# Performance work log

Measured on AMD Instinct MI355X. Metric: run time of the kernel, lower is better.

The kernel has to match this reference:

```python
import jax, jax.numpy as jnp
import numpy as np

DIM = 256
HID = 128


def setup_inputs() -> dict:
    key = jax.random.key(0)
    ks = jax.random.split(key, 10)
    B, T = 8, 2048
    s_in = 1.0 / np.sqrt(DIM)
    s_h = 1.0 / np.sqrt(HID)
    return {
        "x": jax.random.normal(ks[0], (B, T, DIM), jnp.float32),
        "adapt_bias": jax.random.normal(ks[1], (B, T, T), jnp.float32),
        "Wq": jax.random.uniform(ks[2], (HID, DIM), jnp.float32, -s_in, s_in),
        "bq": jax.random.uniform(ks[3], (HID,), jnp.float32, -s_in, s_in),
        "Wk": jax.random.uniform(ks[4], (HID, DIM), jnp.float32, -s_in, s_in),
        "bk": jax.random.uniform(ks[5], (HID,), jnp.float32, -s_in, s_in),
        "Wv": jax.random.uniform(ks[6], (HID, DIM), jnp.float32, -s_in, s_in),
        "bv": jax.random.uniform(ks[7], (HID,), jnp.float32, -s_in, s_in),
        "Wp": jax.random.uniform(ks[8], (DIM, HID), jnp.float32, -s_h, s_h),
        "bp": jax.random.uniform(ks[9], (DIM,), jnp.float32, -s_h, s_h),
    }


def reference(x, adapt_bias, Wq, bq, Wk, bk, Wv, bv, Wp, bp):
    # y = x (default). Q,K,V: [B,T,H]
    Q = jnp.einsum('btd,hd->bth', x, Wq) + bq
    K = jnp.einsum('btd,hd->bth', x, Wk) + bk
    V = jnp.einsum('btd,hd->bth', x, Wv) + bv
    Q_sig = jax.nn.sigmoid(Q)
    ab = jax.nn.softmax(adapt_bias, axis=-1)        # [B,T,T]
    Ksm = jax.nn.softmax(K, axis=1)                 # softmax over time dim
    eab = jnp.exp(ab)                               # [B,T,T]
    eK = jnp.exp(Ksm)                               # [B,T,H]
    num = jnp.einsum('bts,bsh->bth', eab, eK * V)
    den = jnp.einsum('bts,bsh->bth', eab, eK)
    Yt = Q_sig * (num / den)                        # [B,T,H]
    return jnp.einsum('bth,dh->btd', Yt, Wp) + bp   # [B,T,DIM]
```

## Files before the change

### kernel.cpp

```cpp
#include <hip/hip_runtime.h>
#include <hip/hip_bf16.h>

#define B_ 8
#define T_ 2048
#define D_ 256
#define H_ 128

typedef float f32x4 __attribute__((ext_vector_type(4)));
typedef short bf16x8 __attribute__((ext_vector_type(8)));
typedef unsigned short u16x8 __attribute__((ext_vector_type(8)));

__device__ __forceinline__ unsigned short f2bf(float f){
  union { float f; unsigned u; } v; v.f = f;
  unsigned u = v.u;
  unsigned r = (u + 0x7FFFu + ((u >> 16) & 1u)) >> 16;
  return (unsigned short)r;
}

__device__ __forceinline__ float bf2f(unsigned short us){
  union { unsigned u; float f; } v; v.u = ((unsigned)us) << 16; return v.f;
}

#define GLL16(g, l) __builtin_amdgcn_global_load_lds( \
    (const __attribute__((address_space(1))) void*)(g), \
    (__attribute__((address_space(3))) void*)(l), 16, 0, 0)

__device__ __forceinline__ float blk_reduce(float v, bool is_max, float* sbuf){
  for(int o = 32; o > 0; o >>= 1){
    float t = __shfl_xor(v, o);
    v = is_max ? fmaxf(v, t) : (v + t);
  }
  int w = threadIdx.x >> 6;
  __syncthreads();
  if((threadIdx.x & 63) == 0) sbuf[w] = v;
  __syncthreads();
  float r = sbuf[0];
  for(int i = 1; i < 4; i++) r = is_max ? fmaxf(r, sbuf[i]) : (r + sbuf[i]);
  return r;
}

__global__ __launch_bounds__(256) void qkv_kernel(
    const float* __restrict__ x,
    const float* __restrict__ Wq, const float* __restrict__ bq,
    const float* __restrict__ Wk, const float* __restrict__ bk,
    const float* __restrict__ Wv, const float* __restrict__ bv,
    unsigned short* __restrict__ Qsigb, unsigned short* __restrict__ Ktb,
    unsigned short* __restrict__ Vtb)
{
  const int mat = blockIdx.y;
  const int g0  = blockIdx.x * 64;
  const int tid = threadIdx.x;
  const float* W   = (mat == 0) ? Wq : (mat == 1) ? Wk : Wv;
  const float* bia = (mat == 0) ? bq : (mat == 1) ? bk : bv;

  __shared__ __align__(16) short As[64 * 32];
  __shared__ __align__(16) short Ws[128 * 32];
  __shared__ float tbuf[64][129];

  const int w = tid >> 6, lane = tid & 63, rl = lane & 15, kg = lane >> 4;
  f32x4 acc[8];
  for(int i = 0; i < 8; i++) acc[i] = (f32x4){0.f, 0.f, 0.f, 0.f};

  const int c = tid & 31, r8 = tid >> 5;
  for(int kk = 0; kk < 256; kk += 32){
    __syncthreads();
    for(int p = 0; p < 8; p++){
      int rr = r8 + p * 8;
      As[rr * 32 + c] = (short)f2bf(x[(size_t)(g0 + rr) * 256 + kk + c]);
    }
    for(int p = 0; p < 16; p++){
      int hh = r8 + p * 8;
      Ws[hh * 32 + c] = (short)f2bf(W[(size_t)hh * 256 + kk + c]);
    }
    __syncthreads();
    bf16x8 a = *(const bf16x8*)&As[(w * 16 + rl) * 32 + kg * 8];
    for(int cf = 0; cf < 8; cf++){
      bf16x8 bb = *(const bf16x8*)&Ws[(cf * 16 + rl) * 32 + kg * 8];
      acc[cf] = __builtin_amdgcn_mfma_f32_16x16x32_bf16(a, bb, acc[cf], 0, 0, 0);
    }
  }

  const int b = g0 >> 11, t0 = g0 & 2047;
  if(mat == 0){
    for(int cf = 0; cf < 8; cf++){
      int h = cf * 16 + rl;
      float bh = bia[h];
      for(int r = 0; r < 4; r++){
        int tl = w * 16 + kg * 4 + r;
        float v = acc[cf][r] + bh;
        Qsigb[(size_t)(g0 + tl) * 128 + h] = f2bf(1.f / (1.f + __expf(-v)));
      }
    }
  } else {
    for(int cf = 0; cf < 8; cf++){
      int h = cf * 16 + rl;
      float bh = bia[h];
      for(int r = 0; r < 4; r++){
        int tl = w * 16 + kg * 4 + r;
        tbuf[tl][h] = acc[cf][r] + bh;
      }
    }
    __syncthreads();
    unsigned short* dst = (mat == 1) ? Ktb : Vtb;
    int h = tid >> 1, part = tid & 1;
    unsigned short* drow = dst + (size_t)(b * 128 + h) * 2048 + t0 + part * 32;
#pragma unroll
    for(int i = 0; i < 32; i += 8){
      u16x8 o;
#pragma unroll
      for(int j = 0; j < 8; j++) o[j] = f2bf(tbuf[part * 32 + i + j][h]);
      *(u16x8*)(drow + i) = o;
    }
  }
}

__global__ __launch_bounds__(256) void colsm_kernel(
    const unsigned short* __restrict__ Ktb, const unsigned short* __restrict__ Vtb,
    unsigned short* __restrict__ Mt)
{
  __shared__ float sbuf[4];
  const int b  = blockIdx.x >> 5;
  const int hg = blockIdx.x & 31;
  const int tid = threadIdx.x;
  for(int i = 0; i < 4; i++){
    int h = hg * 4 + i;
    const unsigned short* kr = Ktb + (size_t)(b * 128 + h) * 2048;
    const unsigned short* vr = Vtb + (size_t)(b * 128 + h) * 2048;
    u16x8 k8 = *(const u16x8*)(kr + tid * 8);
    u16x8 v8 = *(const u16x8*)(vr + tid * 8);
    float kf[8];
#pragma unroll
    for(int j = 0; j < 8; j++) kf[j] = bf2f(k8[j]);
    float m = kf[0];
#pragma unroll
    for(int j = 1; j < 8; j++) m = fmaxf(m, kf[j]);
    m = blk_reduce(m, true, sbuf);
    float s = 0.f;
#pragma unroll
    for(int j = 0; j < 8; j++) s += __expf(kf[j] - m);
    s = blk_reduce(s, false, sbuf);
    float iz = 1.f / s;
    u16x8 pv, pe;
#pragma unroll
    for(int j = 0; j < 8; j++){
      float e = __expf(__expf(kf[j] - m) * iz);
      pv[j] = f2bf(e * bf2f(v8[j]));
      pe[j] = f2bf(e);
    }
    *(u16x8*)(Mt + (size_t)(b * 256 + h) * 2048 + tid * 8) = pv;
    *(u16x8*)(Mt + (size_t)(b * 256 + 128 + h) * 2048 + tid * 8) = pe;
  }
}

__global__ __launch_bounds__(256) void softexp_kernel(
    const float* __restrict__ ab, unsigned short* __restrict__ eab)
{
  __shared__ float sbuf[4];
  const size_t row = blockIdx.x;
  const float* r = ab + row * 2048;
  const int tid = threadIdx.x;
  float4 v0 = *(const float4*)(r + tid * 4);
  float4 v1 = *(const float4*)(r + tid * 4 + 1024);
  float m = fmaxf(fmaxf(fmaxf(v0.x, v0.y), fmaxf(v0.z, v0.w)),
                  fmaxf(fmaxf(v1.x, v1.y), fmaxf(v1.z, v1.w)));
  m = blk_reduce(m, true, sbuf);
  float e0x = __expf(v0.x - m), e0y = __expf(v0.y - m);
  float e0z = __expf(v0.z - m), e0w = __expf(v0.w - m);
  float e1x = __expf(v1.x - m), e1y = __expf(v1.y - m);
  float e1z = __expf(v1.z - m), e1w = __expf(v1.w - m);
  float s = e0x + e0y + e0z + e0w + e1x + e1y + e1z + e1w;
  s = blk_reduce(s, false, sbuf);
  float iz = 1.f / s;
  ushort4 o;
  o.x = f2bf(__expf(e0x * iz)); o.y = f2bf(__expf(e0y * iz));
  o.z = f2bf(__expf(e0z * iz)); o.w = f2bf(__expf(e0w * iz));
  *(ushort4*)(eab + row * 2048 + tid * 4) = o;
  o.x = f2bf(__expf(e1x * iz)); o.y = f2bf(__expf(e1y * iz));
  o.z = f2bf(__expf(e1z * iz)); o.w = f2bf(__expf(e1w * iz));
  *(ushort4*)(eab + row * 2048 + tid * 4 + 1024) = o;
}

__global__ __launch_bounds__(256) void aft_gemm4(
    const unsigned short* __restrict__ eab,
    const unsigned short* __restrict__ Mt,
    const unsigned short* __restrict__ Qsigb,
    unsigned short* __restrict__ Yt)
{
  __shared__ __align__(16) unsigned short As2[2][64 * 64];
  __shared__ __align__(16) unsigned short Bs2[2][128 * 64];

  const int bid = blockIdx.x;
  const int b   = bid & 7;
  const int idx = bid >> 3;
  const int rt  = idx >> 1;
  const int hb  = idx & 1;
  const int t0  = rt * 64;
  const int h0  = hb * 64;

  const int tid = threadIdx.x;
  const int w = tid >> 6, lane = tid & 63;
  const int rl = lane & 15, kg = lane >> 4;
  const int wr = w >> 1, wc = w & 1;

  const int lr = lane >> 3;
  const int cc = (lane & 7) ^ lr;

  const size_t rowbase = (size_t)b * 2048 + t0;
  const unsigned short* a_src = eab + (rowbase + (size_t)(w * 16 + lr)) * 2048 + cc * 8;
  const int mtrow = (w < 2) ? (h0 + w * 32 + lr) : (128 + h0 + (w - 2) * 32 + lr);
  const unsigned short* b_src = Mt + ((size_t)b * 256 + mtrow) * 2048 + cc * 8;

  f32x4 acc[2][4];
#pragma unroll
  for(int i = 0; i < 2; i++)
#pragma unroll
    for(int j = 0; j < 4; j++) acc[i][j] = (f32x4){0.f, 0.f, 0.f, 0.f};

  auto stage = [&](int buf, int t){
#pragma unroll
    for(int i = 0; i < 2; i++)
      GLL16(a_src + (size_t)i * 8 * 2048 + t * 64, &As2[buf][(w * 16 + i * 8) * 64]);
#pragma unroll
    for(int i = 0; i < 4; i++)
      GLL16(b_src + (size_t)i * 8 * 2048 + t * 64, &Bs2[buf][(w * 32 + i * 8) * 64]);
  };

  const int rx = rl & 7;
  stage(0, 0);
  stage(1, 1);

  for(int t = 0; t < 32; ++t){
    const int cur = t & 1;
    if(t < 31) asm volatile("s_waitcnt vmcnt(6)" ::: "memory");
    else       asm volatile("s_waitcnt vmcnt(0)" ::: "memory");
    __builtin_amdgcn_s_barrier();
    asm volatile("" ::: "memory");

    bf16x8 af[2][2], bfr[2][4];
#pragma unroll
    for(int ks = 0; ks < 2; ++ks){
      const int slot = ((ks * 4 + kg) ^ rx) * 8;
      af[ks][0] = *(const bf16x8*)&As2[cur][(wr * 32 + rl) * 64 + slot];
      af[ks][1] = *(const bf16x8*)&As2[cur][(wr * 32 + 16 + rl) * 64 + slot];
#pragma unroll
      for(int cf = 0; cf < 4; ++cf){
        const int brow = ((cf < 2) ? (wc * 32 + cf * 16)
                                   : (64 + wc * 32 + (cf - 2) * 16)) + rl;
        bfr[ks][cf] = *(const bf16x8*)&Bs2[cur][brow * 64 + slot];
      }
    }
    asm volatile("s_waitcnt lgkmcnt(0)" ::: "memory");
    __builtin_amdgcn_sched_barrier(0);
    __builtin_amdgcn_s_barrier();
    asm volatile("" ::: "memory");

    if(t < 30) stage(cur, t + 2);

    __builtin_amdgcn_s_setprio(1);
#pragma unroll
    for(int ks = 0; ks < 2; ++ks)
#pragma unroll
      for(int cf = 0; cf < 4; ++cf){
        acc[0][cf] = __builtin_amdgcn_mfma_f32_16x16x32_bf16(af[ks][0], bfr[ks][cf], acc[0][cf], 0, 0, 0);
        acc[1][cf] = __builtin_amdgcn_mfma_f32_16x16x32_bf16(af[ks][1], bfr[ks][cf], acc[1][cf], 0, 0, 0);
      }
    __builtin_amdgcn_s_setprio(0);
  }

#pragma unroll
  for(int rf = 0; rf < 2; ++rf)
#pragma unroll
    for(int cf = 0; cf < 2; ++cf){
      const int h = h0 + wc * 32 + cf * 16 + rl;
#pragma unroll
      for(int r = 0; r < 4; ++r){
        const int tl = wr * 32 + rf * 16 + kg * 4 + r;
        const size_t g = rowbase + tl;
        float num = acc[rf][cf][r], den = acc[rf][cf + 2][r];
        float q = bf2f(Qsigb[g * 128 + h]);
        Yt[g * 128 + h] = f2bf(q * num / den);
      }
    }
}

__global__ __launch_bounds__(256) void outproj_kernel(
    const unsigned short* __restrict__ Yt, const float* __restrict__ Wp,
    const float* __restrict__ bp, float* __restrict__ out)
{
  __shared__ __align__(16) short As[64 * 32];
  __shared__ __align__(16) short Bs[256 * 32];
  const int g0 = blockIdx.x * 64;
  const int tid = threadIdx.x;
  const int w = tid >> 6, lane = tid & 63, rl = lane & 15, kg = lane >> 4;
  f32x4 acc[16];
  for(int i = 0; i < 16; i++) acc[i] = (f32x4){0.f, 0.f, 0.f, 0.f};

  const int ar = tid >> 2, apart = tid & 3;
  const int c = tid & 31, dr = tid >> 5;
  for(int k = 0; k < 128; k += 32){
    __syncthreads();
    *(uint4*)&As[ar * 32 + apart * 8] =
        *(const uint4*)(Yt + (size_t)(g0 + ar) * 128 + k + apart * 8);
    for(int p = 0; p < 32; p++){
      int d = dr + p * 8;
      Bs[d * 32 + c] = (short)f2bf(Wp[(size_t)d * 128 + k + c]);
    }
    __syncthreads();
    bf16x8 a = *(const bf16x8*)&As[(w * 16 + rl) * 32 + kg * 8];
    for(int cf = 0; cf < 16; cf++){
      bf16x8 bb = *(const bf16x8*)&Bs[(cf * 16 + rl) * 32 + kg * 8];
      acc[cf] = __builtin_amdgcn_mfma_f32_16x16x32_bf16(a, bb, acc[cf], 0, 0, 0);
    }
  }
  for(int cf = 0; cf < 16; cf++){
    int d = cf * 16 + rl;
    float bpd = bp[d];
    for(int r = 0; r < 4; r++){
      int tl = w * 16 + kg * 4 + r;
      out[(size_t)(g0 + tl) * 256 + d] = acc[cf][r] + bpd;
    }
  }
}

extern "C" void kernel_launch(void* const* d_in, const int* in_sizes, int n_in,
                              void* d_out, int out_size, void* d_ws, size_t ws_size,
                              hipStream_t stream)
{
  const float* x  = (const float*)d_in[0];
  const float* ab = (const float*)d_in[1];
  const float* Wq = (const float*)d_in[2];
  const float* bq = (const float*)d_in[3];
  const float* Wk = (const float*)d_in[4];
  const float* bk = (const float*)d_in[5];
  const float* Wv = (const float*)d_in[6];
  const float* bv = (const float*)d_in[7];
  const float* Wp = (const float*)d_in[8];
  const float* bp = (const float*)d_in[9];
  float* out = (float*)d_out;

  char* ws = (char*)d_ws;
  unsigned short* Qsigb = (unsigned short*)(ws);
  unsigned short* Ktb   = (unsigned short*)(ws + 8388608);
  unsigned short* Vtb   = (unsigned short*)(ws + 12582912);
  unsigned short* Mt    = (unsigned short*)(ws + 16777216);
  unsigned short* eab   = (unsigned short*)(ws + 25165824);
  unsigned short* Yt    = (unsigned short*)(ws + 8388608);

  qkv_kernel<<<dim3(256, 3), 256, 0, stream>>>(x, Wq, bq, Wk, bk, Wv, bv, Qsigb, Ktb, Vtb);
  colsm_kernel<<<256, 256, 0, stream>>>(Ktb, Vtb, Mt);
  softexp_kernel<<<16384, 256, 0, stream>>>(ab, eab);
  aft_gemm4<<<512, 256, 0, stream>>>(eab, Mt, Qsigb, Yt);
  outproj_kernel<<<256, 256, 0, stream>>>(Yt, Wp, bp, out);
}
```

Measured before the change: 92.94 us.

## Load GEMM operands directly from global into registers, dropping LDS staging

The main attention GEMM no longer stages eab and Mt tiles through LDS with async global-to-LDS loads and barriers. Each wave now loads its MFMA fragments straight from global memory into registers, double-buffered in registers across k-steps, and launch bounds request three blocks per SU. This removes LDS traffic and block-wide synchronisation. In exchange, operands shared between waves are fetched from global or L2 more than once, each lane issues 16-byte loads strided across rows, and register pressure rises.

```diff
diff --git a/kernel.cpp b/kernel.cpp
--- a/kernel.cpp
+++ b/kernel.cpp
@@ -20,10 +20,6 @@
 __device__ __forceinline__ float bf2f(unsigned short us){
   union { unsigned u; float f; } v; v.u = ((unsigned)us) << 16; return v.f;
 }
-
-#define GLL16(g, l) __builtin_amdgcn_global_load_lds( \
-    (const __attribute__((address_space(1))) void*)(g), \
-    (__attribute__((address_space(3))) void*)(l), 16, 0, 0)
 
 __device__ __forceinline__ float blk_reduce(float v, bool is_max, float* sbuf){
   for(int o = 32; o > 0; o >>= 1){
@@ -180,15 +176,12 @@
   *(ushort4*)(eab + row * 2048 + tid * 4 + 1024) = o;
 }
 
-__global__ __launch_bounds__(256) void aft_gemm4(
+__global__ __launch_bounds__(256, 3) void aft_gemm10(
     const unsigned short* __restrict__ eab,
     const unsigned short* __restrict__ Mt,
     const unsigned short* __restrict__ Qsigb,
     unsigned short* __restrict__ Yt)
 {
-  __shared__ __align__(16) unsigned short As2[2][64 * 64];
-  __shared__ __align__(16) unsigned short Bs2[2][128 * 64];
-
   const int bid = blockIdx.x;
   const int b   = bid & 7;
   const int idx = bid >> 3;
@@ -202,13 +195,17 @@
   const int rl = lane & 15, kg = lane >> 4;
   const int wr = w >> 1, wc = w & 1;
 
-  const int lr = lane >> 3;
-  const int cc = (lane & 7) ^ lr;
-
   const size_t rowbase = (size_t)b * 2048 + t0;
-  const unsigned short* a_src = eab + (rowbase + (size_t)(w * 16 + lr)) * 2048 + cc * 8;
-  const int mtrow = (w < 2) ? (h0 + w * 32 + lr) : (128 + h0 + (w - 2) * 32 + lr);
-  const unsigned short* b_src = Mt + ((size_t)b * 256 + mtrow) * 2048 + cc * 8;
+
+  const unsigned short* a_base =
+      eab + (rowbase + (size_t)(wr * 32 + rl)) * 2048 + kg * 8;
+  const unsigned short* b_base[4];
+#pragma unroll
+  for(int cf = 0; cf < 4; cf++){
+    const int colbase = (cf < 2) ? (h0 + wc * 32 + cf * 16)
+                                 : (128 + h0 + wc * 32 + (cf - 2) * 16);
+    b_base[cf] = Mt + ((size_t)b * 256 + colbase + rl) * 2048 + kg * 8;
+  }
 
   f32x4 acc[2][4];
 #pragma unroll
@@ -216,56 +213,38 @@
 #pragma unroll
     for(int j = 0; j < 4; j++) acc[i][j] = (f32x4){0.f, 0.f, 0.f, 0.f};
 
-  auto stage = [&](int buf, int t){
-#pragma unroll
-    for(int i = 0; i < 2; i++)
-      GLL16(a_src + (size_t)i * 8 * 2048 + t * 64, &As2[buf][(w * 16 + i * 8) * 64]);
-#pragma unroll
-    for(int i = 0; i < 4; i++)
-      GLL16(b_src + (size_t)i * 8 * 2048 + t * 64, &Bs2[buf][(w * 32 + i * 8) * 64]);
-  };
-
-  const int rx = rl & 7;
-  stage(0, 0);
-  stage(1, 1);
-
-  for(int t = 0; t < 32; ++t){
-    const int cur = t & 1;
-    if(t < 31) asm volatile("s_waitcnt vmcnt(6)" ::: "memory");
-    else       asm volatile("s_waitcnt vmcnt(0)" ::: "memory");
-    __builtin_amdgcn_s_barrier();
-    asm volatile("" ::: "memory");
-
-    bf16x8 af[2][2], bfr[2][4];
-#pragma unroll
-    for(int ks = 0; ks < 2; ++ks){
-      const int slot = ((ks * 4 + kg) ^ rx) * 8;
-      af[ks][0] = *(const bf16x8*)&As2[cur][(wr * 32 + rl) * 64 + slot];
-      af[ks][1] = *(const bf16x8*)&As2[cur][(wr * 32 + 16 + rl) * 64 + slot];
-#pragma unroll
-      for(int cf = 0; cf < 4; ++cf){
-        const int brow = ((cf < 2) ? (wc * 32 + cf * 16)
-                                   : (64 + wc * 32 + (cf - 2) * 16)) + rl;
-        bfr[ks][cf] = *(const bf16x8*)&Bs2[cur][brow * 64 + slot];
-      }
-    }
-    asm volatile("s_waitcnt lgkmcnt(0)" ::: "memory");
-    __builtin_amdgcn_sched_barrier(0);
-    __builtin_amdgcn_s_barrier();
-    asm volatile("" ::: "memory");
-
-    if(t < 30) stage(cur, t + 2);
-
-    __builtin_amdgcn_s_setprio(1);
-#pragma unroll
-    for(int ks = 0; ks < 2; ++ks)
-#pragma unroll
-      for(int cf = 0; cf < 4; ++cf){
-        acc[0][cf] = __builtin_amdgcn_mfma_f32_16x16x32_bf16(af[ks][0], bfr[ks][cf], acc[0][cf], 0, 0, 0);
-        acc[1][cf] = __builtin_amdgcn_mfma_f32_16x16x32_bf16(af[ks][1], bfr[ks][cf], acc[1][cf], 0, 0, 0);
-      }
-    __builtin_amdgcn_s_setprio(0);
-  }
+  #define LOADT(AB, t) do { \
+    _Pragma("unroll") \
+    for(int ks = 0; ks < 2; ++ks){ \
+      AB##A[ks][0] = *(const bf16x8*)(a_base + (t) * 64 + ks * 32); \
+      AB##A[ks][1] = *(const bf16x8*)(a_base + 16 * 2048 + (t) * 64 + ks * 32); \
+      _Pragma("unroll") \
+      for(int cf = 0; cf < 4; ++cf) \
+        AB##B[ks][cf] = *(const bf16x8*)(b_base[cf] + (t) * 64 + ks * 32); \
+    } \
+  } while(0)
+
+  #define MM(AB) do { \
+    _Pragma("unroll") \
+    for(int ks = 0; ks < 2; ++ks) \
+      _Pragma("unroll") \
+      for(int cf = 0; cf < 4; ++cf){ \
+        acc[0][cf] = __builtin_amdgcn_mfma_f32_16x16x32_bf16(AB##A[ks][0], AB##B[ks][cf], acc[0][cf], 0, 0, 0); \
+        acc[1][cf] = __builtin_amdgcn_mfma_f32_16x16x32_bf16(AB##A[ks][1], AB##B[ks][cf], acc[1][cf], 0, 0, 0); \
+      } \
+  } while(0)
+
+  bf16x8 XA[2][2], XB[2][4], YA[2][2], YB[2][4];
+  LOADT(X, 0);
+#pragma unroll 1
+  for(int t = 0; t < 32; t += 2){
+    LOADT(Y, t + 1);
+    MM(X);
+    if(t + 2 < 32) LOADT(X, t + 2);
+    MM(Y);
+  }
+  #undef LOADT
+  #undef MM
 
 #pragma unroll
   for(int rf = 0; rf < 2; ++rf)
@@ -349,6 +328,6 @@
   qkv_kernel<<<dim3(256, 3), 256, 0, stream>>>(x, Wq, bq, Wk, bk, Wv, bv, Qsigb, Ktb, Vtb);
   colsm_kernel<<<256, 256, 0, stream>>>(Ktb, Vtb, Mt);
   softexp_kernel<<<16384, 256, 0, stream>>>(ab, eab);
-  aft_gemm4<<<512, 256, 0, stream>>>(eab, Mt, Qsigb, Yt);
+  aft_gemm10<<<512, 256, 0, stream>>>(eab, Mt, Qsigb, Yt);
   outproj_kernel<<<256, 256, 0, stream>>>(Yt, Wp, bp, out);
 }
```

Measured after the change: 155.8 us. 1.68x slower.

## Software-pipeline LDS fragment reads against MFMA with register double buffering

Applied to the files above, without the earlier changes.

Restructures the main GEMM loop so the LDS reads for the next k-tile go into a second register set while MFMAs run on the current one, with the loop manually unrolled by two to alternate buffers. It also adds a launch-bounds occupancy hint of 3 blocks per CU. The goal is to hide LDS read latency behind matrix math. The cost is a doubled fragment register footprint, which may conflict with the occupancy hint and cause spills.

```diff
diff --git a/kernel.cpp b/kernel.cpp
--- a/kernel.cpp
+++ b/kernel.cpp
@@ -180,7 +180,7 @@
   *(ushort4*)(eab + row * 2048 + tid * 4 + 1024) = o;
 }
 
-__global__ __launch_bounds__(256) void aft_gemm4(
+__global__ __launch_bounds__(256, 3) void aft_gemm11(
     const unsigned short* __restrict__ eab,
     const unsigned short* __restrict__ Mt,
     const unsigned short* __restrict__ Qsigb,
@@ -226,46 +226,72 @@
   };
 
   const int rx = rl & 7;
+
+  #define DSREAD(BK_, cur) do { \
+    _Pragma("unroll") \
+    for(int ks = 0; ks < 2; ++ks){ \
+      const int slot = ((ks * 4 + kg) ^ rx) * 8; \
+      BK_##A[ks][0] = *(const bf16x8*)&As2[cur][(wr * 32 + rl) * 64 + slot]; \
+      BK_##A[ks][1] = *(const bf16x8*)&As2[cur][(wr * 32 + 16 + rl) * 64 + slot]; \
+      _Pragma("unroll") \
+      for(int cf = 0; cf < 4; ++cf){ \
+        const int brow = ((cf < 2) ? (wc * 32 + cf * 16) \
+                                   : (64 + wc * 32 + (cf - 2) * 16)) + rl; \
+        BK_##B[ks][cf] = *(const bf16x8*)&Bs2[cur][brow * 64 + slot]; \
+      } \
+    } \
+  } while(0)
+
+  #define MM(BK_) do { \
+    __builtin_amdgcn_s_setprio(1); \
+    _Pragma("unroll") \
+    for(int ks = 0; ks < 2; ++ks) \
+      _Pragma("unroll") \
+      for(int cf = 0; cf < 4; ++cf){ \
+        acc[0][cf] = __builtin_amdgcn_mfma_f32_16x16x32_bf16(BK_##A[ks][0], BK_##B[ks][cf], acc[0][cf], 0, 0, 0); \
+        acc[1][cf] = __builtin_amdgcn_mfma_f32_16x16x32_bf16(BK_##A[ks][1], BK_##B[ks][cf], acc[1][cf], 0, 0, 0); \
+      } \
+    __builtin_amdgcn_s_setprio(0); \
+  } while(0)
+
+  #define ITER(t, CUR, NXT) do { \
+    if((t) < 30) stage((t) & 1, (t) + 2); \
+    if((t) < 30) asm volatile("s_waitcnt vmcnt(6)" ::: "memory"); \
+    else         asm volatile("s_waitcnt vmcnt(0)" ::: "memory"); \
+    __builtin_amdgcn_s_barrier(); \
+    asm volatile("" ::: "memory"); \
+    DSREAD(NXT, ((t) + 1) & 1); \
+    MM(CUR); \
+    asm volatile("s_waitcnt lgkmcnt(0)" ::: "memory"); \
+    __builtin_amdgcn_sched_barrier(0); \
+    __builtin_amdgcn_s_barrier(); \
+    asm volatile("" ::: "memory"); \
+  } while(0)
+
+  bf16x8 XA[2][2], XB[2][4], YA[2][2], YB[2][4];
+
   stage(0, 0);
   stage(1, 1);
-
-  for(int t = 0; t < 32; ++t){
-    const int cur = t & 1;
-    if(t < 31) asm volatile("s_waitcnt vmcnt(6)" ::: "memory");
-    else       asm volatile("s_waitcnt vmcnt(0)" ::: "memory");
-    __builtin_amdgcn_s_barrier();
-    asm volatile("" ::: "memory");
-
-    bf16x8 af[2][2], bfr[2][4];
-#pragma unroll
-    for(int ks = 0; ks < 2; ++ks){
-      const int slot = ((ks * 4 + kg) ^ rx) * 8;
-      af[ks][0] = *(const bf16x8*)&As2[cur][(wr * 32 + rl) * 64 + slot];
-      af[ks][1] = *(const bf16x8*)&As2[cur][(wr * 32 + 16 + rl) * 64 + slot];
-#pragma unroll
-      for(int cf = 0; cf < 4; ++cf){
-        const int brow = ((cf < 2) ? (wc * 32 + cf * 16)
-                                   : (64 + wc * 32 + (cf - 2) * 16)) + rl;
-        bfr[ks][cf] = *(const bf16x8*)&Bs2[cur][brow * 64 + slot];
-      }
-    }
-    asm volatile("s_waitcnt lgkmcnt(0)" ::: "memory");
-    __builtin_amdgcn_sched_barrier(0);
-    __builtin_amdgcn_s_barrier();
-    asm volatile("" ::: "memory");
-
-    if(t < 30) stage(cur, t + 2);
-
-    __builtin_amdgcn_s_setprio(1);
-#pragma unroll
-    for(int ks = 0; ks < 2; ++ks)
-#pragma unroll
-      for(int cf = 0; cf < 4; ++cf){
-        acc[0][cf] = __builtin_amdgcn_mfma_f32_16x16x32_bf16(af[ks][0], bfr[ks][cf], acc[0][cf], 0, 0, 0);
-        acc[1][cf] = __builtin_amdgcn_mfma_f32_16x16x32_bf16(af[ks][1], bfr[ks][cf], acc[1][cf], 0, 0, 0);
-      }
-    __builtin_amdgcn_s_setprio(0);
-  }
+  asm volatile("s_waitcnt vmcnt(6)" ::: "memory");
+  __builtin_amdgcn_s_barrier();
+  asm volatile("" ::: "memory");
+  DSREAD(X, 0);
+  asm volatile("s_waitcnt lgkmcnt(0)" ::: "memory");
+  __builtin_amdgcn_sched_barrier(0);
+  __builtin_amdgcn_s_barrier();
+  asm volatile("" ::: "memory");
+
+#pragma unroll 1
+  for(int t = 0; t < 30; t += 2){
+    ITER(t,     X, Y);
+    ITER(t + 1, Y, X);
+  }
+  ITER(30, X, Y);
+  MM(Y);
+
+  #undef ITER
+  #undef MM
+  #undef DSREAD
 
 #pragma unroll
   for(int rf = 0; rf < 2; ++rf)
@@ -349,6 +375,6 @@
   qkv_kernel<<<dim3(256, 3), 256, 0, stream>>>(x, Wq, bq, Wk, bk, Wv, bv, Qsigb, Ktb, Vtb);
   colsm_kernel<<<256, 256, 0, stream>>>(Ktb, Vtb, Mt);
   softexp_kernel<<<16384, 256, 0, stream>>>(ab, eab);
-  aft_gemm4<<<512, 256, 0, stream>>>(eab, Mt, Qsigb, Yt);
+  aft_gemm11<<<512, 256, 0, stream>>>(eab, Mt, Qsigb, Yt);
   outproj_kernel<<<256, 256, 0, stream>>>(Yt, Wp, bp, out);
 }
```

After: 96.67 us. 1.04x slower.
